# Kernel tuning notes

Hardware: AMD Instinct MI355X
Metric: run time of the kernel (lower is better)

Reference implementation:

```python
import jax, jax.numpy as jnp
import numpy as np

N = 200000      # active sites
C = 128         # channels (inplanes == planes)
H = W = 1024    # spatial grid for coordinate hashing
K = 9           # 3x3 kernel offsets


def _build_nbr_idx(rng):
    """Rulebook for a 3x3 submanifold conv: nbr_idx[n, k] = row index of the
    active neighbor of site n at kernel offset k, or N (sentinel) if that
    neighbor is inactive or out of grid."""
    lin = rng.choice(H * W, size=N, replace=False).astype(np.int64)
    lookup = np.full(H * W, N, dtype=np.int32)
    lookup[lin] = np.arange(N, dtype=np.int32)
    y, x = lin // W, lin % W
    nbr = np.full((N, K), N, dtype=np.int32)
    k = 0
    for dy in (-1, 0, 1):
        for dx in (-1, 0, 1):
            ny, nx = y + dy, x + dx
            valid = (ny >= 0) & (ny < H) & (nx >= 0) & (nx < W)
            nl = np.where(valid, ny * W + nx, 0)
            nbr[:, k] = np.where(valid, lookup[nl], N)
            k += 1
    return nbr


def setup_inputs() -> dict:
    key = jax.random.key(0)
    k1, k2, k3 = jax.random.split(key, 3)
    rng = np.random.default_rng(0)
    scale = 1.0 / np.sqrt(K * C)
    return {
        "feats": jax.random.normal(k1, (N, C), dtype=jnp.float32),
        "nbr_idx": jnp.asarray(_build_nbr_idx(rng)),
        "W1": jax.random.normal(k2, (K, C, C), dtype=jnp.float32) * scale,
        "W2": jax.random.normal(k3, (K, C, C), dtype=jnp.float32) * scale,
    }


def _subm_conv(f, Wk, nbr_idx):
    # gather-GEMM: pad with a zero row so sentinel index N reads zeros
    fp = jnp.concatenate([f, jnp.zeros((1, f.shape[1]), f.dtype)], axis=0)
    g = fp[nbr_idx]                       # [N, K, Cin]
    return jnp.einsum('nkc,kco->no', g, Wk)  # [N, Cout]


def reference(feats, nbr_idx, W1, W2):
    # out = relu(conv2(relu(conv1(x))) + x), both convs 3x3 submanifold, no bias
    out = jax.nn.relu(_subm_conv(feats, W1, nbr_idx))
    out = _subm_conv(out, W2, nbr_idx)
    return jax.nn.relu(out + feats)
```

## Files before the change

### kernel.cpp

```cpp
#include <hip/hip_runtime.h>

#define CD 128
#define KK 9

typedef __bf16 bf16x8 __attribute__((ext_vector_type(8)));
typedef float  f32x4  __attribute__((ext_vector_type(4)));
typedef float  f32x16 __attribute__((ext_vector_type(16)));

typedef __attribute__((address_space(1))) const void* gas_ptr;
typedef __attribute__((address_space(3))) void*       las_ptr;

__global__ __launch_bounds__(256) void cast_feats(const float* __restrict__ src,
                                                  unsigned short* __restrict__ dst,
                                                  const long total8) {
    const long stride = (long)gridDim.x * 256;
    for (long i = (long)blockIdx.x * 256 + threadIdx.x; i < total8; i += stride) {
        f32x4 lo = *(const f32x4*)(src + i * 8);
        f32x4 hi = *(const f32x4*)(src + i * 8 + 4);
        bf16x8 v;
        #pragma unroll
        for (int e = 0; e < 4; ++e) {
            v[e]     = (__bf16)lo[e];
            v[e + 4] = (__bf16)hi[e];
        }
        *(bf16x8*)(dst + i * 8) = v;
    }
}

__global__ __launch_bounds__(256) void transpose_w(const float* __restrict__ W1,
                                                   const float* __restrict__ W2,
                                                   unsigned short* __restrict__ W1T,
                                                   unsigned short* __restrict__ W2T) {
    __shared__ unsigned short tile[128 * 129];
    const int b = blockIdx.x;
    const int k = (b < KK) ? b : b - KK;
    const float* src = ((b < KK) ? W1 : W2) + k * (CD * CD);
    unsigned short* dst = ((b < KK) ? W1T : W2T) + k * (CD * CD);
    #pragma unroll 4
    for (int p = 0; p < 64; ++p) {
        int idx = p * 256 + threadIdx.x;
        int c = idx >> 7, o = idx & 127;
        __bf16 h = (__bf16)src[idx];
        tile[o * 129 + c] = __builtin_bit_cast(unsigned short, h);
    }
    __syncthreads();
    #pragma unroll 4
    for (int p = 0; p < 64; ++p) {
        int idx = p * 256 + threadIdx.x;
        int o = idx >> 7, c = idx & 127;
        dst[idx] = tile[o * 129 + c];
    }
}

template <bool FIRST>
__device__ __forceinline__ void conv_body(
    const unsigned short* __restrict__ asrc,
    const float* __restrict__ resid,
    const unsigned short* __restrict__ WT,
    const int* __restrict__ nbr,
    unsigned short* __restrict__ hout,
    float* __restrict__ fout,
    const int n, char (*wbuf)[32768])
{
    const int tid  = threadIdx.x;
    const int lane = tid & 63;
    const int l31  = lane & 31;
    const int kh   = lane >> 5;
    const int wave = tid >> 6;
    const int base = blockIdx.x * 256 + wave * 64;
    const int s0 = base + l31;
    const int s1 = base + 32 + l31;
    const int sc0 = (s0 < n) ? s0 : (n - 1);
    const int sc1 = (s1 < n) ? s1 : (n - 1);

    auto stage = [&](int b, int k) {
        const char* tap = (const char*)(WT + (size_t)k * CD * CD);
        char* lb = &wbuf[b][0];
        #pragma unroll
        for (int i = 0; i < 8; ++i) {
            const int chunk = (i * 4 + wave) * 1024;
            const int d = chunk + lane * 16;
            const int s = d ^ (((d >> 8) & 7) << 4);
            __builtin_amdgcn_global_load_lds((gas_ptr)(tap + s),
                                             (las_ptr)(lb + chunk), 16, 0, 0);
        }
    };

    f32x16 acc[2][4];
    #pragma unroll
    for (int m = 0; m < 2; ++m)
        #pragma unroll
        for (int nf = 0; nf < 4; ++nf)
            #pragma unroll
            for (int i = 0; i < 16; ++i) acc[m][nf][i] = 0.f;

    bf16x8 zed;
    #pragma unroll
    for (int e = 0; e < 8; ++e) zed[e] = (__bf16)0.f;

    int c0 = nbr[(size_t)sc0 * KK];
    int c1 = nbr[(size_t)sc1 * KK];
    stage(0, 0);
    __syncthreads();

    const int swq = (l31 & 7) << 4;

    #pragma unroll 1
    for (int k = 0; k < KK; ++k) {
        int n0 = 0, n1 = 0;
        if (k + 1 < KK) {
            n0 = nbr[(size_t)sc0 * KK + k + 1];
            n1 = nbr[(size_t)sc1 * KK + k + 1];
            stage((k + 1) & 1, k + 1);
        }

        const bool v0 = (unsigned)c0 < (unsigned)n;
        const bool v1 = (unsigned)c1 < (unsigned)n;
        const size_t rr0 = (size_t)(v0 ? c0 : 0) * CD;
        const size_t rr1 = (size_t)(v1 ? c1 : 0) * CD;

        bf16x8 a0[8], a1[8];
        #pragma unroll
        for (int cs = 0; cs < 8; ++cs) {
            const int coff = cs * 16 + kh * 8;
            a0[cs] = *(const bf16x8*)(asrc + rr0 + coff);
            a1[cs] = *(const bf16x8*)(asrc + rr1 + coff);
            a0[cs] = v0 ? a0[cs] : zed;
            a1[cs] = v1 ? a1[cs] : zed;
        }

        const char* wb = &wbuf[k & 1][0];
        #pragma unroll
        for (int cs = 0; cs < 8; ++cs) {
            #pragma unroll
            for (int nf = 0; nf < 4; ++nf) {
                const int x = ((nf * 32 + l31) << 8) + (cs << 5) + (kh << 4);
                bf16x8 b = *(const bf16x8*)(wb + (x ^ swq));
                acc[0][nf] = __builtin_amdgcn_mfma_f32_32x32x16_bf16(a0[cs], b, acc[0][nf], 0, 0, 0);
                acc[1][nf] = __builtin_amdgcn_mfma_f32_32x32x16_bf16(a1[cs], b, acc[1][nf], 0, 0, 0);
            }
        }

        __syncthreads();
        c0 = n0; c1 = n1;
    }

    #pragma unroll
    for (int m = 0; m < 2; ++m) {
        #pragma unroll
        for (int rg = 0; rg < 16; ++rg) {
            const int row  = (rg & 3) + 8 * (rg >> 2) + 4 * kh;
            const int srow = base + m * 32 + row;
            if (srow < n) {
                #pragma unroll
                for (int nf = 0; nf < 4; ++nf) {
                    float v = acc[m][nf][rg];
                    const size_t oi = (size_t)srow * CD + nf * 32 + l31;
                    if (FIRST) {
                        v = v > 0.f ? v : 0.f;
                        hout[oi] = __builtin_bit_cast(unsigned short, (__bf16)v);
                    } else {
                        v += resid[oi];
                        v = v > 0.f ? v : 0.f;
                        fout[oi] = v;
                    }
                }
            }
        }
    }
}

__global__ __launch_bounds__(256, 2) void conv1_kernel(
    const unsigned short* __restrict__ fb16,
    const unsigned short* __restrict__ WT,
    const int* __restrict__ nbr,
    unsigned short* __restrict__ hout,
    const int n)
{
    __shared__ __align__(16) char wbuf[2][32768];
    conv_body<true>(fb16, nullptr, WT, nbr, hout, nullptr, n, wbuf);
}

__global__ __launch_bounds__(256, 2) void conv2_kernel(
    const unsigned short* __restrict__ hid,
    const float* __restrict__ feats,
    const unsigned short* __restrict__ WT,
    const int* __restrict__ nbr,
    float* __restrict__ fout,
    const int n)
{
    __shared__ __align__(16) char wbuf[2][32768];
    conv_body<false>(hid, feats, WT, nbr, nullptr, fout, n, wbuf);
}

extern "C" void kernel_launch(void* const* d_in, const int* in_sizes, int n_in,
                              void* d_out, int out_size, void* d_ws, size_t ws_size,
                              hipStream_t stream) {
    const float* feats = (const float*)d_in[0];
    const int*   nbr   = (const int*)d_in[1];
    const float* W1    = (const float*)d_in[2];
    const float* W2    = (const float*)d_in[3];
    float* out = (float*)d_out;

    const int n = in_sizes[0] / CD;

    unsigned short* hid  = (unsigned short*)d_ws;
    unsigned short* W1T  = hid + (size_t)n * CD;
    unsigned short* W2T  = W1T + KK * CD * CD;
    unsigned short* fb16 = W2T + KK * CD * CD;
    const size_t need = ((size_t)n * CD * 2 + (size_t)2 * KK * CD * CD) * 2;
    if (ws_size < need) {
        fb16 = (unsigned short*)d_out;
    }

    const long total8 = (long)n * CD / 8;
    cast_feats<<<2048, 256, 0, stream>>>(feats, fb16, total8);
    transpose_w<<<2 * KK, 256, 0, stream>>>(W1, W2, W1T, W2T);

    const int grid = (n + 255) / 256;
    conv1_kernel<<<grid, 256, 0, stream>>>(fb16, W1T, nbr, hid, n);
    conv2_kernel<<<grid, 256, 0, stream>>>(hid, feats, W2T, nbr, out, n);
}
```

Before: 219.2 us.

## Merge prep kernels, preload residual into accumulators, reorder gathers, use nontemporal I/O

Merges the feature cast and weight transpose into one prep launch, which removes one kernel launch. In conv2 the accumulators start from the residual, loaded with nontemporal loads while the first weight tap is staged, so the epilogue no longer reads the residual. The output is written with nontemporal stores. Inside the k loop, the activation gathers are now issued before the next tap's neighbor-index load and weight staging. The trade-off is that the residual preload adds register pressure and memory traffic at kernel start.

```diff
diff --git a/kernel.cpp b/kernel.cpp
--- a/kernel.cpp
+++ b/kernel.cpp
@@ -10,45 +10,46 @@
 typedef __attribute__((address_space(1))) const void* gas_ptr;
 typedef __attribute__((address_space(3))) void*       las_ptr;
 
-__global__ __launch_bounds__(256) void cast_feats(const float* __restrict__ src,
-                                                  unsigned short* __restrict__ dst,
-                                                  const long total8) {
-    const long stride = (long)gridDim.x * 256;
-    for (long i = (long)blockIdx.x * 256 + threadIdx.x; i < total8; i += stride) {
-        f32x4 lo = *(const f32x4*)(src + i * 8);
-        f32x4 hi = *(const f32x4*)(src + i * 8 + 4);
-        bf16x8 v;
-        #pragma unroll
-        for (int e = 0; e < 4; ++e) {
-            v[e]     = (__bf16)lo[e];
-            v[e + 4] = (__bf16)hi[e];
-        }
-        *(bf16x8*)(dst + i * 8) = v;
-    }
-}
-
-__global__ __launch_bounds__(256) void transpose_w(const float* __restrict__ W1,
-                                                   const float* __restrict__ W2,
-                                                   unsigned short* __restrict__ W1T,
-                                                   unsigned short* __restrict__ W2T) {
-    __shared__ unsigned short tile[128 * 129];
-    const int b = blockIdx.x;
-    const int k = (b < KK) ? b : b - KK;
-    const float* src = ((b < KK) ? W1 : W2) + k * (CD * CD);
-    unsigned short* dst = ((b < KK) ? W1T : W2T) + k * (CD * CD);
-    #pragma unroll 4
-    for (int p = 0; p < 64; ++p) {
-        int idx = p * 256 + threadIdx.x;
-        int c = idx >> 7, o = idx & 127;
-        __bf16 h = (__bf16)src[idx];
-        tile[o * 129 + c] = __builtin_bit_cast(unsigned short, h);
-    }
-    __syncthreads();
-    #pragma unroll 4
-    for (int p = 0; p < 64; ++p) {
-        int idx = p * 256 + threadIdx.x;
-        int o = idx >> 7, c = idx & 127;
-        dst[idx] = tile[o * 129 + c];
+#define CAST_BLOCKS 2030
+__global__ __launch_bounds__(256) void prep_kernel(
+    const float* __restrict__ feats, unsigned short* __restrict__ fb16,
+    const float* __restrict__ W1, const float* __restrict__ W2,
+    unsigned short* __restrict__ W1T, unsigned short* __restrict__ W2T,
+    const long total8) {
+    if (blockIdx.x < 2 * KK) {
+        __shared__ unsigned short tile[128 * 129];
+        const int b = blockIdx.x;
+        const int k = (b < KK) ? b : b - KK;
+        const float* src = ((b < KK) ? W1 : W2) + k * (CD * CD);
+        unsigned short* dst = ((b < KK) ? W1T : W2T) + k * (CD * CD);
+        #pragma unroll 4
+        for (int p = 0; p < 64; ++p) {
+            int idx = p * 256 + threadIdx.x;
+            int c = idx >> 7, o = idx & 127;
+            __bf16 h = (__bf16)src[idx];
+            tile[o * 129 + c] = __builtin_bit_cast(unsigned short, h);
+        }
+        __syncthreads();
+        #pragma unroll 4
+        for (int p = 0; p < 64; ++p) {
+            int idx = p * 256 + threadIdx.x;
+            int o = idx >> 7, c = idx & 127;
+            dst[idx] = tile[o * 129 + c];
+        }
+    } else {
+        const long stride = (long)CAST_BLOCKS * 256;
+        for (long i = (long)(blockIdx.x - 2 * KK) * 256 + threadIdx.x;
+             i < total8; i += stride) {
+            f32x4 lo = *(const f32x4*)(feats + i * 8);
+            f32x4 hi = *(const f32x4*)(feats + i * 8 + 4);
+            bf16x8 v;
+            #pragma unroll
+            for (int e = 0; e < 4; ++e) {
+                v[e]     = (__bf16)lo[e];
+                v[e + 4] = (__bf16)hi[e];
+            }
+            *(bf16x8*)(fb16 + i * 8) = v;
+        }
     }
 }
 
@@ -87,33 +88,46 @@
     };
 
     f32x16 acc[2][4];
-    #pragma unroll
-    for (int m = 0; m < 2; ++m)
-        #pragma unroll
-        for (int nf = 0; nf < 4; ++nf)
-            #pragma unroll
-            for (int i = 0; i < 16; ++i) acc[m][nf][i] = 0.f;
+    if (FIRST) {
+        #pragma unroll
+        for (int m = 0; m < 2; ++m)
+            #pragma unroll
+            for (int nf = 0; nf < 4; ++nf)
+                #pragma unroll
+                for (int i = 0; i < 16; ++i) acc[m][nf][i] = 0.f;
+    }
+
+    int c0 = nbr[(size_t)sc0 * KK];
+    int c1 = nbr[(size_t)sc1 * KK];
+    stage(0, 0);
+
+    if (!FIRST) {
+        #pragma unroll
+        for (int m = 0; m < 2; ++m)
+            #pragma unroll
+            for (int rg = 0; rg < 16; ++rg) {
+                const int row  = (rg & 3) + 8 * (rg >> 2) + 4 * kh;
+                const int srow = base + m * 32 + row;
+                #pragma unroll
+                for (int nf = 0; nf < 4; ++nf) {
+                    float r = 0.f;
+                    if (srow < n)
+                        r = __builtin_nontemporal_load(
+                                resid + (size_t)srow * CD + nf * 32 + l31);
+                    acc[m][nf][rg] = r;
+                }
+            }
+    }
+    __syncthreads();
 
     bf16x8 zed;
     #pragma unroll
     for (int e = 0; e < 8; ++e) zed[e] = (__bf16)0.f;
 
-    int c0 = nbr[(size_t)sc0 * KK];
-    int c1 = nbr[(size_t)sc1 * KK];
-    stage(0, 0);
-    __syncthreads();
-
     const int swq = (l31 & 7) << 4;
 
     #pragma unroll 1
     for (int k = 0; k < KK; ++k) {
-        int n0 = 0, n1 = 0;
-        if (k + 1 < KK) {
-            n0 = nbr[(size_t)sc0 * KK + k + 1];
-            n1 = nbr[(size_t)sc1 * KK + k + 1];
-            stage((k + 1) & 1, k + 1);
-        }
-
         const bool v0 = (unsigned)c0 < (unsigned)n;
         const bool v1 = (unsigned)c1 < (unsigned)n;
         const size_t rr0 = (size_t)(v0 ? c0 : 0) * CD;
@@ -127,6 +141,13 @@
             a1[cs] = *(const bf16x8*)(asrc + rr1 + coff);
             a0[cs] = v0 ? a0[cs] : zed;
             a1[cs] = v1 ? a1[cs] : zed;
+        }
+
+        int n0 = 0, n1 = 0;
+        if (k + 1 < KK) {
+            n0 = nbr[(size_t)sc0 * KK + k + 1];
+            n1 = nbr[(size_t)sc1 * KK + k + 1];
+            stage((k + 1) & 1, k + 1);
         }
 
         const char* wb = &wbuf[k & 1][0];
@@ -155,14 +176,12 @@
                 #pragma unroll
                 for (int nf = 0; nf < 4; ++nf) {
                     float v = acc[m][nf][rg];
+                    v = v > 0.f ? v : 0.f;
                     const size_t oi = (size_t)srow * CD + nf * 32 + l31;
                     if (FIRST) {
-                        v = v > 0.f ? v : 0.f;
                         hout[oi] = __builtin_bit_cast(unsigned short, (__bf16)v);
                     } else {
-                        v += resid[oi];
-                        v = v > 0.f ? v : 0.f;
-                        fout[oi] = v;
+                        __builtin_nontemporal_store(v, fout + oi);
                     }
                 }
             }
@@ -214,8 +233,8 @@
     }
 
     const long total8 = (long)n * CD / 8;
-    cast_feats<<<2048, 256, 0, stream>>>(feats, fb16, total8);
-    transpose_w<<<2 * KK, 256, 0, stream>>>(W1, W2, W1T, W2T);
+    prep_kernel<<<2 * KK + CAST_BLOCKS, 256, 0, stream>>>(
+        feats, fb16, W1, W2, W1T, W2T, total8);
 
     const int grid = (n + 255) / 256;
     conv1_kernel<<<grid, 256, 0, stream>>>(fb16, W1T, nbr, hid, n);
```

Result: slower. 225.3 us (+2.8%).
